# Optimization experiments

Hardware: AMD Instinct MI355X
Metric: run time of the kernel (lower is better)

The kernel has to match this reference:

```python
import jax, jax.numpy as jnp
import numpy as np

N_X, N_NEIGH, D_IN, D_HID, D_OUT = 8192, 8192, 512, 32, 256
NEG_BIG = -9.0e15


def setup_inputs() -> dict:
    key = jax.random.key(0)
    ks = jax.random.split(key, 16)
    s_in = 1.0 / np.sqrt(D_IN)
    s_hid = 1.0 / np.sqrt(D_HID)
    return {
        "x": jax.random.normal(ks[0], (N_X, D_IN), jnp.float32),
        "neigh": jax.random.normal(ks[1], (N_NEIGH, D_IN), jnp.float32),
        "adj": jax.random.randint(ks[2], (N_X, N_NEIGH), 0, 2, jnp.int32),
        # att_x MLP: Linear(D_IN,D_HID) -> tanh -> Linear(D_HID,D_HID)
        "Wx1": jax.random.uniform(ks[3], (D_IN, D_HID), jnp.float32, -s_in, s_in),
        "bx1": jnp.zeros((D_HID,), jnp.float32),
        "Wx2": jax.random.uniform(ks[4], (D_HID, D_HID), jnp.float32, -s_hid, s_hid),
        "bx2": jnp.zeros((D_HID,), jnp.float32),
        # att_neigh MLP
        "Wn1": jax.random.uniform(ks[5], (D_IN, D_HID), jnp.float32, -s_in, s_in),
        "bn1": jnp.zeros((D_HID,), jnp.float32),
        "Wn2": jax.random.uniform(ks[6], (D_HID, D_HID), jnp.float32, -s_hid, s_hid),
        "bn2": jnp.zeros((D_HID,), jnp.float32),
        # fc_value, fc_x
        "Wv": jax.random.uniform(ks[7], (D_IN, D_OUT), jnp.float32, -s_in, s_in),
        "bv": jnp.zeros((D_OUT,), jnp.float32),
        "Wfx": jax.random.uniform(ks[8], (D_IN, D_OUT), jnp.float32, -s_in, s_in),
        "bfx": jnp.zeros((D_OUT,), jnp.float32),
    }


def reference(x, neigh, adj, Wx1, bx1, Wx2, bx2, Wn1, bn1, Wn2, bn2, Wv, bv, Wfx, bfx):
    # eval mode: dropouts are identity. edge_emb gather in original is dead code.
    neib_att = jnp.tanh(neigh @ Wn1 + bn1) @ Wn2 + bn2      # (N_neigh, H)
    value = neigh @ Wv + bv                                  # (N_neigh, D_OUT)
    x_att = jnp.tanh(x @ Wx1 + bx1) @ Wx2 + bx2              # (N_x, H)
    ws = jnp.einsum("nh,mh->nm", x_att, neib_att)            # (N_x, N_neigh)
    ws = jax.nn.leaky_relu(ws, negative_slope=0.01)
    ws = jnp.where(adj > 0, ws, jnp.float32(NEG_BIG))
    ws = jax.nn.softmax(ws, axis=1)
    agg_neib = ws @ value                                    # (N_x, D_OUT)
    out = jnp.concatenate([x @ Wfx + bfx, agg_neib], axis=1)  # (N_x, 2*D_OUT)
    return out
```

## Files before the change

kernel.cpp:

```cpp
#include <hip/hip_runtime.h>
#include <hip/hip_bf16.h>

#define NX 8192
#define NN 8192
#define DIN 512
#define DHID 32
#define DOUT 256

typedef __bf16 bf16x8 __attribute__((ext_vector_type(8)));
typedef float f32x4 __attribute__((ext_vector_type(4)));
typedef unsigned short u16x8 __attribute__((ext_vector_type(8)));

__device__ __forceinline__ unsigned short f2bf(float f) {
  __hip_bfloat16 h = __float2bfloat16(f);
  return __builtin_bit_cast(unsigned short, h);
}
__device__ __forceinline__ float bf2f(unsigned short u) {
  unsigned int v = ((unsigned int)u) << 16;
  return __builtin_bit_cast(float, v);
}
__device__ __forceinline__ f32x4 mfma16(u16x8 a, u16x8 b, f32x4 c) {
  return __builtin_amdgcn_mfma_f32_16x16x32_bf16(
      __builtin_bit_cast(bf16x8, a), __builtin_bit_cast(bf16x8, b), c, 0, 0, 0);
}
__device__ __forceinline__ u16x8 cvt8(float4 a0, float4 a1) {
  u16x8 u;
  u[0] = f2bf(a0.x); u[1] = f2bf(a0.y); u[2] = f2bf(a0.z); u[3] = f2bf(a0.w);
  u[4] = f2bf(a1.x); u[5] = f2bf(a1.y); u[6] = f2bf(a1.z); u[7] = f2bf(a1.w);
  return u;
}

__global__ __launch_bounds__(256) void k_wt(
    const float* __restrict__ Wv, const float* __restrict__ Wfx,
    const float* __restrict__ Wx1, const float* __restrict__ Wn1,
    const float* __restrict__ Wx2, const float* __restrict__ Wn2,
    unsigned short* __restrict__ WvT, unsigned short* __restrict__ WfxT,
    unsigned short* __restrict__ Wx1T, unsigned short* __restrict__ Wn1T,
    unsigned short* __restrict__ Wx2T, unsigned short* __restrict__ Wn2T) {
  const float* src; unsigned short* dst; int C, n;
  switch (blockIdx.y) {
    case 0:  src = Wv;  dst = WvT;  C = 256; n = DIN * 256; break;
    case 1:  src = Wfx; dst = WfxT; C = 256; n = DIN * 256; break;
    case 2:  src = Wx1; dst = Wx1T; C = 32;  n = DIN * 32;  break;
    case 3:  src = Wn1; dst = Wn1T; C = 32;  n = DIN * 32;  break;
    case 4:  src = Wx2; dst = Wx2T; C = 32;  n = 32 * 32;   break;
    default: src = Wn2; dst = Wn2T; C = 32;  n = 32 * 32;   break;
  }
  int idx = blockIdx.x * 256 + threadIdx.x;
  if (idx >= n) return;
  int K = n / C;
  int k = idx / C, c = idx % C;
  dst[c * K + k] = f2bf(src[idx]);
}

__global__ __launch_bounds__(256) void k_hidden(
    const float* __restrict__ x, const float* __restrict__ neigh,
    const float* __restrict__ bx1, const float* __restrict__ bn1,
    const unsigned short* __restrict__ Wx1T, const unsigned short* __restrict__ Wn1T,
    unsigned short* __restrict__ Hx, unsigned short* __restrict__ Hn) {
  const float* A; const float* b1; const unsigned short* WT; unsigned short* H;
  if (blockIdx.y == 0) { A = x; b1 = bx1; WT = Wx1T; H = Hx; }
  else                 { A = neigh; b1 = bn1; WT = Wn1T; H = Hn; }
  int lane = threadIdx.x & 63, w = threadIdx.x >> 6;
  int r = lane & 15, h4 = lane >> 4;
  int row = blockIdx.x * 64 + w * 16 + r;
  const float* ap = A + (long)row * DIN;
  f32x4 acc0 = {0.f, 0.f, 0.f, 0.f}, acc1 = {0.f, 0.f, 0.f, 0.f};
  for (int kk = 0; kk < 16; ++kk) {
    int k0 = kk * 32 + h4 * 8;
    float4 a0 = *reinterpret_cast<const float4*>(ap + k0);
    float4 a1 = *reinterpret_cast<const float4*>(ap + k0 + 4);
    u16x8 af = cvt8(a0, a1);
    u16x8 bf0 = *reinterpret_cast<const u16x8*>(WT + r * DIN + k0);
    u16x8 bf1 = *reinterpret_cast<const u16x8*>(WT + (16 + r) * DIN + k0);
    acc0 = mfma16(af, bf0, acc0);
    acc1 = mfma16(af, bf1, acc1);
  }
  int orow = blockIdx.x * 64 + w * 16 + h4 * 4;
  #pragma unroll
  for (int j = 0; j < 4; ++j) {
    H[(orow + j) * DHID + r]      = f2bf(tanhf(acc0[j] + b1[r]));
    H[(orow + j) * DHID + 16 + r] = f2bf(tanhf(acc1[j] + b1[16 + r]));
  }
}

__global__ __launch_bounds__(256) void k_att(
    const unsigned short* __restrict__ Hx, const unsigned short* __restrict__ Hn,
    const float* __restrict__ bx2, const float* __restrict__ bn2,
    const unsigned short* __restrict__ Wx2T, const unsigned short* __restrict__ Wn2T,
    unsigned short* __restrict__ xatt, unsigned short* __restrict__ natt) {
  const unsigned short* H; const float* b2; const unsigned short* WT; unsigned short* att;
  if (blockIdx.y == 0) { H = Hx; b2 = bx2; WT = Wx2T; att = xatt; }
  else                 { H = Hn; b2 = bn2; WT = Wn2T; att = natt; }
  int lane = threadIdx.x & 63, w = threadIdx.x >> 6;
  int r = lane & 15, h4 = lane >> 4;
  int row = blockIdx.x * 64 + w * 16 + r;
  u16x8 af = *reinterpret_cast<const u16x8*>(H + row * DHID + h4 * 8);
  u16x8 b0 = *reinterpret_cast<const u16x8*>(WT + r * DHID + h4 * 8);
  u16x8 b1 = *reinterpret_cast<const u16x8*>(WT + (16 + r) * DHID + h4 * 8);
  f32x4 z = {0.f, 0.f, 0.f, 0.f};
  f32x4 acc0 = mfma16(af, b0, z);
  f32x4 acc1 = mfma16(af, b1, z);
  int orow = blockIdx.x * 64 + w * 16 + h4 * 4;
  #pragma unroll
  for (int j = 0; j < 4; ++j) {
    att[(orow + j) * DHID + r]      = f2bf(acc0[j] + b2[r]);
    att[(orow + j) * DHID + 16 + r] = f2bf(acc1[j] + b2[16 + r]);
  }
}

__global__ __launch_bounds__(256) void k_vfc(
    const float* __restrict__ x, const float* __restrict__ neigh,
    const float* __restrict__ bfx, const float* __restrict__ bv,
    const unsigned short* __restrict__ WfxT, const unsigned short* __restrict__ WvT,
    float* __restrict__ out, unsigned short* __restrict__ Vp) {
  int job = blockIdx.y;
  const float* A = job ? neigh : x;
  const float* bias = job ? bv : bfx;
  const unsigned short* WT = job ? WvT : WfxT;
  __shared__ __align__(16) char As[64 * 64];
  int t = threadIdx.x;
  int lane = t & 63, w = t >> 6;
  int r = lane & 15, h4 = lane >> 4;
  int bm = blockIdx.x * 64;
  f32x4 acc[4][4];
  #pragma unroll
  for (int i = 0; i < 4; ++i)
    #pragma unroll
    for (int j = 0; j < 4; ++j) acc[i][j] = (f32x4){0.f, 0.f, 0.f, 0.f};
  int srow = t >> 2, kq = t & 3;
  const float* ap = A + (long)(bm + srow) * DIN + kq * 8;
  for (int kk = 0; kk < 16; ++kk) {
    float4 a0 = *reinterpret_cast<const float4*>(ap + kk * 32);
    float4 a1 = *reinterpret_cast<const float4*>(ap + kk * 32 + 4);
    u16x8 u = cvt8(a0, a1);
    int boff = (srow * 64 + kq * 16) ^ ((srow & 3) << 4);
    *reinterpret_cast<u16x8*>(As + boff) = u;
    __syncthreads();
    u16x8 pb[4];
    #pragma unroll
    for (int nt = 0; nt < 4; ++nt)
      pb[nt] = *reinterpret_cast<const u16x8*>(WT + (w * 64 + nt * 16 + r) * DIN + kk * 32 + h4 * 8);
    #pragma unroll
    for (int mt = 0; mt < 4; ++mt) {
      int ro = mt * 16 + r;
      int aoff = (ro * 64 + h4 * 16) ^ ((ro & 3) << 4);
      u16x8 pa = *reinterpret_cast<const u16x8*>(As + aoff);
      #pragma unroll
      for (int nt = 0; nt < 4; ++nt) acc[mt][nt] = mfma16(pa, pb[nt], acc[mt][nt]);
    }
    __syncthreads();
  }
  #pragma unroll
  for (int mt = 0; mt < 4; ++mt)
    #pragma unroll
    for (int nt = 0; nt < 4; ++nt) {
      int c = w * 64 + nt * 16 + r;
      #pragma unroll
      for (int j = 0; j < 4; ++j) {
        int row = bm + mt * 16 + h4 * 4 + j;
        float v = acc[mt][nt][j] + bias[c];
        if (job == 0) out[(long)row * 512 + c] = v;
        else Vp[((row >> 3) * 256 + c) * 8 + (row & 7)] = f2bf(v);
      }
    }
}

__global__ __launch_bounds__(256) void k_flash(
    const int* __restrict__ adj, const unsigned short* __restrict__ xatt,
    const unsigned short* __restrict__ natt, const unsigned short* __restrict__ Vp,
    float* __restrict__ out, float* __restrict__ accP, float* __restrict__ lP, int nc) {
  __shared__ unsigned short P[32 * 72];
  __shared__ float lsum[32];
  int t = threadIdx.x;
  if (t < 32) lsum[t] = 0.f;
  int lane = t & 63, w = t >> 6;
  int r = lane & 15, h4 = lane >> 4;
  int rb = blockIdx.x * 32;
  int L = NN / nc;
  int base = blockIdx.y * L;
  int NIT = L / 64;
  u16x8 qf0 = *reinterpret_cast<const u16x8*>(xatt + (rb + r) * DHID + h4 * 8);
  u16x8 qf1 = *reinterpret_cast<const u16x8*>(xatt + (rb + 16 + r) * DHID + h4 * 8);
  f32x4 o[2][4];
  #pragma unroll
  for (int i = 0; i < 2; ++i)
    #pragma unroll
    for (int j = 0; j < 4; ++j) o[i][j] = (f32x4){0.f, 0.f, 0.f, 0.f};
  int acur[8];
  #pragma unroll
  for (int rt = 0; rt < 2; ++rt)
    #pragma unroll
    for (int j = 0; j < 4; ++j)
      acur[rt * 4 + j] = adj[(long)(rb + rt * 16 + h4 * 4 + j) * NN + base + w * 16 + r];
  __syncthreads();
  for (int it = 0; it < NIT; ++it) {
    int n0 = base + it * 64;
    u16x8 kf = *reinterpret_cast<const u16x8*>(natt + (n0 + w * 16 + r) * DHID + h4 * 8);
    f32x4 z = {0.f, 0.f, 0.f, 0.f};
    f32x4 s0 = mfma16(qf0, kf, z);
    f32x4 s1 = mfma16(qf1, kf, z);
    int anext[8];
    int nn0 = (it + 1 < NIT) ? (n0 + 64) : n0;
    #pragma unroll
    for (int rt = 0; rt < 2; ++rt)
      #pragma unroll
      for (int j = 0; j < 4; ++j)
        anext[rt * 4 + j] = adj[(long)(rb + rt * 16 + h4 * 4 + j) * NN + nn0 + w * 16 + r];
    #pragma unroll
    for (int rt = 0; rt < 2; ++rt) {
      f32x4 s = rt ? s1 : s0;
      #pragma unroll
      for (int j = 0; j < 4; ++j) {
        float sv = s[j];
        float lr = fminf(fmaxf(sv, 0.01f * sv), 60.f);
        float p = (acur[rt * 4 + j] > 0) ? __expf(lr) : 0.f;
        P[(rt * 16 + h4 * 4 + j) * 72 + w * 16 + r] = f2bf(p);
      }
    }
    #pragma unroll
    for (int q = 0; q < 8; ++q) acur[q] = anext[q];
    __syncthreads();
    {
      int trow = t >> 3, tq = t & 7;
      u16x8 pv = *reinterpret_cast<const u16x8*>(P + trow * 72 + tq * 8);
      float s8 = 0.f;
      #pragma unroll
      for (int i = 0; i < 8; ++i) s8 += bf2f(pv[i]);
      s8 += __shfl_xor(s8, 1);
      s8 += __shfl_xor(s8, 2);
      s8 += __shfl_xor(s8, 4);
      if (tq == 0) lsum[trow] += s8;
    }
    #pragma unroll
    for (int kb = 0; kb < 2; ++kb) {
      u16x8 pa0 = *reinterpret_cast<const u16x8*>(P + r * 72 + kb * 32 + h4 * 8);
      u16x8 pa1 = *reinterpret_cast<const u16x8*>(P + (16 + r) * 72 + kb * 32 + h4 * 8);
      long vbase = ((long)((n0 + kb * 32) >> 3) + h4) * (DOUT * 8);
      #pragma unroll
      for (int nt = 0; nt < 4; ++nt) {
        u16x8 vf = *reinterpret_cast<const u16x8*>(Vp + vbase + (w * 64 + nt * 16 + r) * 8);
        o[0][nt] = mfma16(pa0, vf, o[0][nt]);
        o[1][nt] = mfma16(pa1, vf, o[1][nt]);
      }
    }
    __syncthreads();
  }
  if (nc == 1) {
    #pragma unroll
    for (int rt = 0; rt < 2; ++rt)
      #pragma unroll
      for (int nt = 0; nt < 4; ++nt) {
        int c = w * 64 + nt * 16 + r;
        #pragma unroll
        for (int j = 0; j < 4; ++j) {
          int rl = rt * 16 + h4 * 4 + j;
          out[(long)(rb + rl) * 512 + 256 + c] = o[rt][nt][j] / lsum[rl];
        }
      }
  } else {
    long cb = (long)blockIdx.y * NX;
    #pragma unroll
    for (int rt = 0; rt < 2; ++rt)
      #pragma unroll
      for (int nt = 0; nt < 4; ++nt) {
        int c = w * 64 + nt * 16 + r;
        #pragma unroll
        for (int j = 0; j < 4; ++j) {
          int rl = rt * 16 + h4 * 4 + j;
          accP[(cb + rb + rl) * DOUT + c] = o[rt][nt][j];
        }
      }
    if (t < 32) lP[blockIdx.y * NX + rb + t] = lsum[t];
  }
}

__global__ __launch_bounds__(256) void k_combine(
    const float* __restrict__ accP, const float* __restrict__ lP,
    float* __restrict__ out, int nc) {
  long idx = (long)blockIdx.x * 256 + threadIdx.x;
  int row = (int)(idx >> 8), c = (int)(idx & 255);
  float s = 0.f, l = 0.f;
  for (int q = 0; q < nc; ++q) {
    s += accP[(long)q * NX * DOUT + idx];
    l += lP[q * NX + row];
  }
  out[(long)row * 512 + 256 + c] = s / l;
}

extern "C" void kernel_launch(void* const* d_in, const int* in_sizes, int n_in,
                              void* d_out, int out_size, void* d_ws, size_t ws_size,
                              hipStream_t stream) {
  const float* x    = (const float*)d_in[0];
  const float* neigh= (const float*)d_in[1];
  const int*   adj  = (const int*)d_in[2];
  const float* Wx1  = (const float*)d_in[3];
  const float* bx1  = (const float*)d_in[4];
  const float* Wx2  = (const float*)d_in[5];
  const float* bx2  = (const float*)d_in[6];
  const float* Wn1  = (const float*)d_in[7];
  const float* bn1  = (const float*)d_in[8];
  const float* Wn2  = (const float*)d_in[9];
  const float* bn2  = (const float*)d_in[10];
  const float* Wv   = (const float*)d_in[11];
  const float* bv   = (const float*)d_in[12];
  const float* Wfx  = (const float*)d_in[13];
  const float* bfx  = (const float*)d_in[14];
  float* out = (float*)d_out;
  char* ws = (char*)d_ws;

  unsigned short* xatt = (unsigned short*)(ws + 0);
  unsigned short* natt = (unsigned short*)(ws + 524288);
  unsigned short* Hx   = (unsigned short*)(ws + 1048576);
  unsigned short* Hn   = (unsigned short*)(ws + 1572864);
  unsigned short* Vp   = (unsigned short*)(ws + 2097152);
  unsigned short* WvT  = (unsigned short*)(ws + 6291456);
  unsigned short* WfxT = (unsigned short*)(ws + 6553600);
  unsigned short* Wx1T = (unsigned short*)(ws + 6815744);
  unsigned short* Wn1T = (unsigned short*)(ws + 6848512);
  unsigned short* Wx2T = (unsigned short*)(ws + 6881280);
  unsigned short* Wn2T = (unsigned short*)(ws + 6883328);

  const size_t OFF_ACC = 8388608;
  const size_t CHUNK_ACC = (size_t)NX * DOUT * 4;
  size_t need4 = OFF_ACC + 4 * CHUNK_ACC + 4 * NX * 4;
  size_t need2 = OFF_ACC + 2 * CHUNK_ACC + 2 * NX * 4;
  int nc = (ws_size >= need4) ? 4 : (ws_size >= need2) ? 2 : 1;
  float* accP = (float*)(ws + OFF_ACC);
  float* lP   = (float*)(ws + OFF_ACC + (size_t)nc * CHUNK_ACC);

  k_wt<<<dim3(512, 6), 256, 0, stream>>>(Wv, Wfx, Wx1, Wn1, Wx2, Wn2,
                                         WvT, WfxT, Wx1T, Wn1T, Wx2T, Wn2T);
  k_hidden<<<dim3(128, 2), 256, 0, stream>>>(x, neigh, bx1, bn1, Wx1T, Wn1T, Hx, Hn);
  k_att<<<dim3(128, 2), 256, 0, stream>>>(Hx, Hn, bx2, bn2, Wx2T, Wn2T, xatt, natt);
  k_vfc<<<dim3(128, 2), 256, 0, stream>>>(x, neigh, bfx, bv, WfxT, WvT, out, Vp);
  k_flash<<<dim3(256, nc), 256, 0, stream>>>(adj, xatt, natt, Vp, out, accP, lP, nc);
  if (nc > 1)
    k_combine<<<dim3(NX * DOUT / 256), 256, 0, stream>>>(accP, lP, out, nc);
}
```

Before: 565.9 us.

## Fuse hidden and value GEMMs, double-buffer flash P tile, bf16 partials

After: 520.9 us. 8.0% less time.

```diff
diff --git a/kernel.cpp b/kernel.cpp
--- a/kernel.cpp
+++ b/kernel.cpp
@@ -37,50 +37,126 @@
     unsigned short* __restrict__ WvT, unsigned short* __restrict__ WfxT,
     unsigned short* __restrict__ Wx1T, unsigned short* __restrict__ Wn1T,
     unsigned short* __restrict__ Wx2T, unsigned short* __restrict__ Wn2T) {
-  const float* src; unsigned short* dst; int C, n;
+  const float* src; unsigned short* dst; int K, C;
   switch (blockIdx.y) {
-    case 0:  src = Wv;  dst = WvT;  C = 256; n = DIN * 256; break;
-    case 1:  src = Wfx; dst = WfxT; C = 256; n = DIN * 256; break;
-    case 2:  src = Wx1; dst = Wx1T; C = 32;  n = DIN * 32;  break;
-    case 3:  src = Wn1; dst = Wn1T; C = 32;  n = DIN * 32;  break;
-    case 4:  src = Wx2; dst = Wx2T; C = 32;  n = 32 * 32;   break;
-    default: src = Wn2; dst = Wn2T; C = 32;  n = 32 * 32;   break;
-  }
-  int idx = blockIdx.x * 256 + threadIdx.x;
-  if (idx >= n) return;
-  int K = n / C;
-  int k = idx / C, c = idx % C;
-  dst[c * K + k] = f2bf(src[idx]);
-}
-
-__global__ __launch_bounds__(256) void k_hidden(
+    case 0:  src = Wv;  dst = WvT;  K = DIN; C = 256; break;
+    case 1:  src = Wfx; dst = WfxT; K = DIN; C = 256; break;
+    case 2:  src = Wx1; dst = Wx1T; K = DIN; C = 32;  break;
+    case 3:  src = Wn1; dst = Wn1T; K = DIN; C = 32;  break;
+    case 4:  src = Wx2; dst = Wx2T; K = 32;  C = 32;  break;
+    default: src = Wn2; dst = Wn2T; K = 32;  C = 32;  break;
+  }
+  int tc = C >> 5, tk = K >> 5;
+  if ((int)blockIdx.x >= tc * tk) return;
+  int ik = blockIdx.x / tc, ic = blockIdx.x % tc;
+  __shared__ float tile[32][33];
+  int t = threadIdx.x, tx = t & 31, ty0 = t >> 5;
+  #pragma unroll
+  for (int q = 0; q < 4; ++q) {
+    int ty = ty0 + q * 8;
+    tile[ty][tx] = src[(ik * 32 + ty) * C + ic * 32 + tx];
+  }
+  __syncthreads();
+  #pragma unroll
+  for (int q = 0; q < 4; ++q) {
+    int ty = ty0 + q * 8;
+    dst[(ic * 32 + ty) * K + ik * 32 + tx] = f2bf(tile[tx][ty]);
+  }
+}
+
+__global__ __launch_bounds__(256) void k_prep(
     const float* __restrict__ x, const float* __restrict__ neigh,
+    const float* __restrict__ bfx, const float* __restrict__ bv,
     const float* __restrict__ bx1, const float* __restrict__ bn1,
+    const unsigned short* __restrict__ WfxT, const unsigned short* __restrict__ WvT,
     const unsigned short* __restrict__ Wx1T, const unsigned short* __restrict__ Wn1T,
+    float* __restrict__ out, unsigned short* __restrict__ Vp,
     unsigned short* __restrict__ Hx, unsigned short* __restrict__ Hn) {
-  const float* A; const float* b1; const unsigned short* WT; unsigned short* H;
-  if (blockIdx.y == 0) { A = x; b1 = bx1; WT = Wx1T; H = Hx; }
-  else                 { A = neigh; b1 = bn1; WT = Wn1T; H = Hn; }
-  int lane = threadIdx.x & 63, w = threadIdx.x >> 6;
+  int job = blockIdx.y;
+  const float* A = job ? neigh : x;
+  const float* bias = job ? bv : bfx;
+  const float* b1 = job ? bn1 : bx1;
+  const unsigned short* WT = job ? WvT : WfxT;
+  const unsigned short* W1T = job ? Wn1T : Wx1T;
+  unsigned short* H = job ? Hn : Hx;
+  __shared__ __align__(16) char As[2][64 * 64];
+  int t = threadIdx.x;
+  int lane = t & 63, w = t >> 6;
   int r = lane & 15, h4 = lane >> 4;
-  int row = blockIdx.x * 64 + w * 16 + r;
-  const float* ap = A + (long)row * DIN;
-  f32x4 acc0 = {0.f, 0.f, 0.f, 0.f}, acc1 = {0.f, 0.f, 0.f, 0.f};
+  int bm = blockIdx.x * 64;
+  f32x4 acc[4][4];
+  f32x4 acch[4];
+  #pragma unroll
+  for (int i = 0; i < 4; ++i) {
+    acch[i] = (f32x4){0.f, 0.f, 0.f, 0.f};
+    #pragma unroll
+    for (int j = 0; j < 4; ++j) acc[i][j] = (f32x4){0.f, 0.f, 0.f, 0.f};
+  }
+  int srow = t >> 2, kq = t & 3;
+  const float* ap = A + (long)(bm + srow) * DIN + kq * 8;
+  float4 a0 = *reinterpret_cast<const float4*>(ap);
+  float4 a1 = *reinterpret_cast<const float4*>(ap + 4);
+  u16x8 pbc[4], pbhc;
+  #pragma unroll
+  for (int nt = 0; nt < 4; ++nt)
+    pbc[nt] = *reinterpret_cast<const u16x8*>(WT + (w * 64 + nt * 16 + r) * DIN + h4 * 8);
+  if (w < 2)
+    pbhc = *reinterpret_cast<const u16x8*>(W1T + (w * 16 + r) * DIN + h4 * 8);
+  int boff = (srow * 64 + kq * 16) ^ ((srow & 3) << 4);
+  int buf = 0;
   for (int kk = 0; kk < 16; ++kk) {
-    int k0 = kk * 32 + h4 * 8;
-    float4 a0 = *reinterpret_cast<const float4*>(ap + k0);
-    float4 a1 = *reinterpret_cast<const float4*>(ap + k0 + 4);
-    u16x8 af = cvt8(a0, a1);
-    u16x8 bf0 = *reinterpret_cast<const u16x8*>(WT + r * DIN + k0);
-    u16x8 bf1 = *reinterpret_cast<const u16x8*>(WT + (16 + r) * DIN + k0);
-    acc0 = mfma16(af, bf0, acc0);
-    acc1 = mfma16(af, bf1, acc1);
-  }
-  int orow = blockIdx.x * 64 + w * 16 + h4 * 4;
-  #pragma unroll
-  for (int j = 0; j < 4; ++j) {
-    H[(orow + j) * DHID + r]      = f2bf(tanhf(acc0[j] + b1[r]));
-    H[(orow + j) * DHID + 16 + r] = f2bf(tanhf(acc1[j] + b1[16 + r]));
+    u16x8 u = cvt8(a0, a1);
+    *reinterpret_cast<u16x8*>(&As[buf][0] + boff) = u;
+    __syncthreads();
+    u16x8 pbn[4], pbhn;
+    if (kk < 15) {
+      a0 = *reinterpret_cast<const float4*>(ap + (kk + 1) * 32);
+      a1 = *reinterpret_cast<const float4*>(ap + (kk + 1) * 32 + 4);
+      #pragma unroll
+      for (int nt = 0; nt < 4; ++nt)
+        pbn[nt] = *reinterpret_cast<const u16x8*>(
+            WT + (w * 64 + nt * 16 + r) * DIN + (kk + 1) * 32 + h4 * 8);
+      if (w < 2)
+        pbhn = *reinterpret_cast<const u16x8*>(
+            W1T + (w * 16 + r) * DIN + (kk + 1) * 32 + h4 * 8);
+    }
+    #pragma unroll
+    for (int mt = 0; mt < 4; ++mt) {
+      int ro = mt * 16 + r;
+      int aoff = (ro * 64 + h4 * 16) ^ ((ro & 3) << 4);
+      u16x8 pa = *reinterpret_cast<const u16x8*>(&As[buf][0] + aoff);
+      #pragma unroll
+      for (int nt = 0; nt < 4; ++nt) acc[mt][nt] = mfma16(pa, pbc[nt], acc[mt][nt]);
+      if (w < 2) acch[mt] = mfma16(pa, pbhc, acch[mt]);
+    }
+    #pragma unroll
+    for (int nt = 0; nt < 4; ++nt) pbc[nt] = pbn[nt];
+    pbhc = pbhn;
+    buf ^= 1;
+  }
+  #pragma unroll
+  for (int mt = 0; mt < 4; ++mt)
+    #pragma unroll
+    for (int nt = 0; nt < 4; ++nt) {
+      int c = w * 64 + nt * 16 + r;
+      #pragma unroll
+      for (int j = 0; j < 4; ++j) {
+        int row = bm + mt * 16 + h4 * 4 + j;
+        float v = acc[mt][nt][j] + bias[c];
+        if (job == 0) out[(long)row * 512 + c] = v;
+        else Vp[((row >> 3) * 256 + c) * 8 + (row & 7)] = f2bf(v);
+      }
+    }
+  if (w < 2) {
+    int c = w * 16 + r;
+    float bb = b1[c];
+    #pragma unroll
+    for (int mt = 0; mt < 4; ++mt)
+      #pragma unroll
+      for (int j = 0; j < 4; ++j) {
+        int row = bm + mt * 16 + h4 * 4 + j;
+        H[row * DHID + c] = f2bf(tanhf(acch[mt][j] + bb));
+      }
   }
 }
 
@@ -109,71 +185,14 @@
   }
 }
 
-__global__ __launch_bounds__(256) void k_vfc(
-    const float* __restrict__ x, const float* __restrict__ neigh,
-    const float* __restrict__ bfx, const float* __restrict__ bv,
-    const unsigned short* __restrict__ WfxT, const unsigned short* __restrict__ WvT,
-    float* __restrict__ out, unsigned short* __restrict__ Vp) {
-  int job = blockIdx.y;
-  const float* A = job ? neigh : x;
-  const float* bias = job ? bv : bfx;
-  const unsigned short* WT = job ? WvT : WfxT;
-  __shared__ __align__(16) char As[64 * 64];
-  int t = threadIdx.x;
-  int lane = t & 63, w = t >> 6;
-  int r = lane & 15, h4 = lane >> 4;
-  int bm = blockIdx.x * 64;
-  f32x4 acc[4][4];
-  #pragma unroll
-  for (int i = 0; i < 4; ++i)
-    #pragma unroll
-    for (int j = 0; j < 4; ++j) acc[i][j] = (f32x4){0.f, 0.f, 0.f, 0.f};
-  int srow = t >> 2, kq = t & 3;
-  const float* ap = A + (long)(bm + srow) * DIN + kq * 8;
-  for (int kk = 0; kk < 16; ++kk) {
-    float4 a0 = *reinterpret_cast<const float4*>(ap + kk * 32);
-    float4 a1 = *reinterpret_cast<const float4*>(ap + kk * 32 + 4);
-    u16x8 u = cvt8(a0, a1);
-    int boff = (srow * 64 + kq * 16) ^ ((srow & 3) << 4);
-    *reinterpret_cast<u16x8*>(As + boff) = u;
-    __syncthreads();
-    u16x8 pb[4];
-    #pragma unroll
-    for (int nt = 0; nt < 4; ++nt)
-      pb[nt] = *reinterpret_cast<const u16x8*>(WT + (w * 64 + nt * 16 + r) * DIN + kk * 32 + h4 * 8);
-    #pragma unroll
-    for (int mt = 0; mt < 4; ++mt) {
-      int ro = mt * 16 + r;
-      int aoff = (ro * 64 + h4 * 16) ^ ((ro & 3) << 4);
-      u16x8 pa = *reinterpret_cast<const u16x8*>(As + aoff);
-      #pragma unroll
-      for (int nt = 0; nt < 4; ++nt) acc[mt][nt] = mfma16(pa, pb[nt], acc[mt][nt]);
-    }
-    __syncthreads();
-  }
-  #pragma unroll
-  for (int mt = 0; mt < 4; ++mt)
-    #pragma unroll
-    for (int nt = 0; nt < 4; ++nt) {
-      int c = w * 64 + nt * 16 + r;
-      #pragma unroll
-      for (int j = 0; j < 4; ++j) {
-        int row = bm + mt * 16 + h4 * 4 + j;
-        float v = acc[mt][nt][j] + bias[c];
-        if (job == 0) out[(long)row * 512 + c] = v;
-        else Vp[((row >> 3) * 256 + c) * 8 + (row & 7)] = f2bf(v);
-      }
-    }
-}
-
-__global__ __launch_bounds__(256) void k_flash(
+__global__ __launch_bounds__(256, 4) void k_flash(
     const int* __restrict__ adj, const unsigned short* __restrict__ xatt,
     const unsigned short* __restrict__ natt, const unsigned short* __restrict__ Vp,
-    float* __restrict__ out, float* __restrict__ accP, float* __restrict__ lP, int nc) {
-  __shared__ unsigned short P[32 * 72];
-  __shared__ float lsum[32];
+    float* __restrict__ out, unsigned short* __restrict__ accP,
+    float* __restrict__ lP, int nc) {
+  __shared__ unsigned short P[2][32 * 72];
+  __shared__ float lpart[4][32];
   int t = threadIdx.x;
-  if (t < 32) lsum[t] = 0.f;
   int lane = t & 63, w = t >> 6;
   int r = lane & 15, h4 = lane >> 4;
   int rb = blockIdx.x * 32;
@@ -187,26 +206,31 @@
   for (int i = 0; i < 2; ++i)
     #pragma unroll
     for (int j = 0; j < 4; ++j) o[i][j] = (f32x4){0.f, 0.f, 0.f, 0.f};
+  float psum[8];
+  #pragma unroll
+  for (int i = 0; i < 8; ++i) psum[i] = 0.f;
   int acur[8];
   #pragma unroll
   for (int rt = 0; rt < 2; ++rt)
     #pragma unroll
     for (int j = 0; j < 4; ++j)
       acur[rt * 4 + j] = adj[(long)(rb + rt * 16 + h4 * 4 + j) * NN + base + w * 16 + r];
-  __syncthreads();
+  u16x8 kfc = *reinterpret_cast<const u16x8*>(natt + (base + w * 16 + r) * DHID + h4 * 8);
+  int buf = 0;
   for (int it = 0; it < NIT; ++it) {
     int n0 = base + it * 64;
-    u16x8 kf = *reinterpret_cast<const u16x8*>(natt + (n0 + w * 16 + r) * DHID + h4 * 8);
-    f32x4 z = {0.f, 0.f, 0.f, 0.f};
-    f32x4 s0 = mfma16(qf0, kf, z);
-    f32x4 s1 = mfma16(qf1, kf, z);
+    int nn0 = (it + 1 < NIT) ? (n0 + 64) : n0;
     int anext[8];
-    int nn0 = (it + 1 < NIT) ? (n0 + 64) : n0;
     #pragma unroll
     for (int rt = 0; rt < 2; ++rt)
       #pragma unroll
       for (int j = 0; j < 4; ++j)
         anext[rt * 4 + j] = adj[(long)(rb + rt * 16 + h4 * 4 + j) * NN + nn0 + w * 16 + r];
+    u16x8 kfn = *reinterpret_cast<const u16x8*>(natt + (nn0 + w * 16 + r) * DHID + h4 * 8);
+    f32x4 z = {0.f, 0.f, 0.f, 0.f};
+    f32x4 s0 = mfma16(qf0, kfc, z);
+    f32x4 s1 = mfma16(qf1, kfc, z);
+    unsigned short* Pb = &P[buf][0];
     #pragma unroll
     for (int rt = 0; rt < 2; ++rt) {
       f32x4 s = rt ? s1 : s0;
@@ -215,27 +239,15 @@
         float sv = s[j];
         float lr = fminf(fmaxf(sv, 0.01f * sv), 60.f);
         float p = (acur[rt * 4 + j] > 0) ? __expf(lr) : 0.f;
-        P[(rt * 16 + h4 * 4 + j) * 72 + w * 16 + r] = f2bf(p);
-      }
-    }
-    #pragma unroll
-    for (int q = 0; q < 8; ++q) acur[q] = anext[q];
+        psum[rt * 4 + j] += p;
+        Pb[(rt * 16 + h4 * 4 + j) * 72 + w * 16 + r] = f2bf(p);
+      }
+    }
     __syncthreads();
-    {
-      int trow = t >> 3, tq = t & 7;
-      u16x8 pv = *reinterpret_cast<const u16x8*>(P + trow * 72 + tq * 8);
-      float s8 = 0.f;
-      #pragma unroll
-      for (int i = 0; i < 8; ++i) s8 += bf2f(pv[i]);
-      s8 += __shfl_xor(s8, 1);
-      s8 += __shfl_xor(s8, 2);
-      s8 += __shfl_xor(s8, 4);
-      if (tq == 0) lsum[trow] += s8;
-    }
     #pragma unroll
     for (int kb = 0; kb < 2; ++kb) {
-      u16x8 pa0 = *reinterpret_cast<const u16x8*>(P + r * 72 + kb * 32 + h4 * 8);
-      u16x8 pa1 = *reinterpret_cast<const u16x8*>(P + (16 + r) * 72 + kb * 32 + h4 * 8);
+      u16x8 pa0 = *reinterpret_cast<const u16x8*>(Pb + r * 72 + kb * 32 + h4 * 8);
+      u16x8 pa1 = *reinterpret_cast<const u16x8*>(Pb + (16 + r) * 72 + kb * 32 + h4 * 8);
       long vbase = ((long)((n0 + kb * 32) >> 3) + h4) * (DOUT * 8);
       #pragma unroll
       for (int nt = 0; nt < 4; ++nt) {
@@ -244,8 +256,23 @@
         o[1][nt] = mfma16(pa1, vf, o[1][nt]);
       }
     }
-    __syncthreads();
-  }
+    #pragma unroll
+    for (int q = 0; q < 8; ++q) acur[q] = anext[q];
+    kfc = kfn;
+    buf ^= 1;
+  }
+  #pragma unroll
+  for (int q = 1; q < 16; q <<= 1)
+    #pragma unroll
+    for (int i = 0; i < 8; ++i) psum[i] += __shfl_xor(psum[i], q);
+  if (r == 0) {
+    #pragma unroll
+    for (int rt = 0; rt < 2; ++rt)
+      #pragma unroll
+      for (int j = 0; j < 4; ++j)
+        lpart[w][rt * 16 + h4 * 4 + j] = psum[rt * 4 + j];
+  }
+  __syncthreads();
   if (nc == 1) {
     #pragma unroll
     for (int rt = 0; rt < 2; ++rt)
@@ -255,7 +282,8 @@
         #pragma unroll
         for (int j = 0; j < 4; ++j) {
           int rl = rt * 16 + h4 * 4 + j;
-          out[(long)(rb + rl) * 512 + 256 + c] = o[rt][nt][j] / lsum[rl];
+          float l = lpart[0][rl] + lpart[1][rl] + lpart[2][rl] + lpart[3][rl];
+          out[(long)(rb + rl) * 512 + 256 + c] = o[rt][nt][j] / l;
         }
       }
   } else {
@@ -268,21 +296,23 @@
         #pragma unroll
         for (int j = 0; j < 4; ++j) {
           int rl = rt * 16 + h4 * 4 + j;
-          accP[(cb + rb + rl) * DOUT + c] = o[rt][nt][j];
+          accP[(cb + rb + rl) * DOUT + c] = f2bf(o[rt][nt][j]);
         }
       }
-    if (t < 32) lP[blockIdx.y * NX + rb + t] = lsum[t];
+    if (t < 32)
+      lP[blockIdx.y * NX + rb + t] =
+          lpart[0][t] + lpart[1][t] + lpart[2][t] + lpart[3][t];
   }
 }
 
 __global__ __launch_bounds__(256) void k_combine(
-    const float* __restrict__ accP, const float* __restrict__ lP,
+    const unsigned short* __restrict__ accP, const float* __restrict__ lP,
     float* __restrict__ out, int nc) {
   long idx = (long)blockIdx.x * 256 + threadIdx.x;
   int row = (int)(idx >> 8), c = (int)(idx & 255);
   float s = 0.f, l = 0.f;
   for (int q = 0; q < nc; ++q) {
-    s += accP[(long)q * NX * DOUT + idx];
+    s += bf2f(accP[(long)q * NX * DOUT + idx]);
     l += lP[q * NX + row];
   }
   out[(long)row * 512 + 256 + c] = s / l;
@@ -321,19 +351,19 @@
   unsigned short* Wx2T = (unsigned short*)(ws + 6881280);
   unsigned short* Wn2T = (unsigned short*)(ws + 6883328);
 
-  const size_t OFF_ACC = 8388608;
-  const size_t CHUNK_ACC = (size_t)NX * DOUT * 4;
-  size_t need4 = OFF_ACC + 4 * CHUNK_ACC + 4 * NX * 4;
-  size_t need2 = OFF_ACC + 2 * CHUNK_ACC + 2 * NX * 4;
+  const size_t OFF_ACC = 7340032;
+  const size_t CHUNK_ACC = (size_t)NX * DOUT * 2;
+  size_t need4 = OFF_ACC + 4 * (CHUNK_ACC + (size_t)NX * 4);
+  size_t need2 = OFF_ACC + 2 * (CHUNK_ACC + (size_t)NX * 4);
   int nc = (ws_size >= need4) ? 4 : (ws_size >= need2) ? 2 : 1;
-  float* accP = (float*)(ws + OFF_ACC);
-  float* lP   = (float*)(ws + OFF_ACC + (size_t)nc * CHUNK_ACC);
-
-  k_wt<<<dim3(512, 6), 256, 0, stream>>>(Wv, Wfx, Wx1, Wn1, Wx2, Wn2,
+  unsigned short* accP = (unsigned short*)(ws + OFF_ACC);
+  float* lP = (float*)(ws + OFF_ACC + (size_t)nc * CHUNK_ACC);
+
+  k_wt<<<dim3(128, 6), 256, 0, stream>>>(Wv, Wfx, Wx1, Wn1, Wx2, Wn2,
                                          WvT, WfxT, Wx1T, Wn1T, Wx2T, Wn2T);
-  k_hidden<<<dim3(128, 2), 256, 0, stream>>>(x, neigh, bx1, bn1, Wx1T, Wn1T, Hx, Hn);
+  k_prep<<<dim3(128, 2), 256, 0, stream>>>(x, neigh, bfx, bv, bx1, bn1,
+                                           WfxT, WvT, Wx1T, Wn1T, out, Vp, Hx, Hn);
   k_att<<<dim3(128, 2), 256, 0, stream>>>(Hx, Hn, bx2, bn2, Wx2T, Wn2T, xatt, natt);
-  k_vfc<<<dim3(128, 2), 256, 0, stream>>>(x, neigh, bfx, bv, WfxT, WvT, out, Vp);
   k_flash<<<dim3(256, nc), 256, 0, stream>>>(adj, xatt, natt, Vp, out, accP, lP, nc);
   if (nc > 1)
     k_combine<<<dim3(NX * DOUT / 256), 256, 0, stream>>>(accP, lP, out, nc);
```
